# Performance work log

Measured on AMD Instinct MI355X. Metric: run time of the kernel, lower is better.

The kernel has to match this reference:

```python
import jax, jax.numpy as jnp
import numpy as np

N_RAYS = 131072
N_NODES = 524288
ENC_DEPTH = 8
ENC_DIM = 16
N_POINTS = 8
IN_DIM = N_POINTS * ENC_DEPTH * ENC_DIM  # 1024
INNER = 64


def setup_inputs() -> dict:
    key = jax.random.key(0)
    ks = jax.random.split(key, 9)
    orig = jax.random.uniform(ks[0], (N_RAYS, 3), dtype=jnp.float32)
    end = jax.random.uniform(ks[1], (N_RAYS, 3), dtype=jnp.float32)
    history = jax.random.randint(ks[2], (N_RAYS, ENC_DEPTH), 0, N_NODES, dtype=jnp.int32).astype(jnp.int64)
    nodes_min = jax.random.uniform(ks[3], (N_NODES, 3), dtype=jnp.float32)
    # extents strictly positive (module replaces 0 extents with 0.5)
    nodes_extent = jax.random.uniform(ks[4], (N_NODES, 3), dtype=jnp.float32) + 0.1
    emb = jax.random.normal(ks[5], (N_NODES, 8 * ENC_DIM), dtype=jnp.float32) * 0.1
    W1 = jax.random.normal(ks[6], (IN_DIM, INNER), dtype=jnp.float32) * (1.0 / np.sqrt(IN_DIM))
    W2 = jax.random.normal(ks[7], (INNER, INNER), dtype=jnp.float32) * (1.0 / np.sqrt(INNER))
    W3 = jax.random.normal(ks[8], (INNER, 2), dtype=jnp.float32) * (1.0 / np.sqrt(INNER))
    return {"orig": orig, "end": end, "history": history, "nodes_min": nodes_min,
            "nodes_extent": nodes_extent, "emb": emb, "W1": W1, "W2": W2, "W3": W3}


def _net_forward(orig, end, history, nodes_min, nodes_extent, emb, W1, W2, W3):
    n = orig.shape[0]
    d = history.shape[1]
    # gather per-ray, per-depth node data (irregular access)
    nmin = nodes_min[history]          # (n, d, 3)
    ext = nodes_extent[history]        # (n, d, 3)
    po = jnp.clip((orig[:, None, :] - nmin) / ext, 0.0, 1.0)  # (n, d, 3)
    pe = jnp.clip((end[:, None, :] - nmin) / ext, 0.0, 1.0)
    ts = jnp.linspace(0.0, 1.0, N_POINTS, dtype=orig.dtype)
    pts = po[:, :, None, :] + (pe - po)[:, :, None, :] * ts[None, None, :, None]  # (n, d, P, 3)
    xd, yd, zd = pts[..., 0], pts[..., 1], pts[..., 2]
    # corner weights in the same order as bbox_feature.chunk(8): 000,100,010,001,101,011,110,111
    w = jnp.stack([
        (1 - xd) * (1 - yd) * (1 - zd),
        xd * (1 - yd) * (1 - zd),
        (1 - xd) * yd * (1 - zd),
        (1 - xd) * (1 - yd) * zd,
        xd * (1 - yd) * zd,
        (1 - xd) * yd * zd,
        xd * yd * (1 - zd),
        xd * yd * zd,
    ], axis=-1)                                    # (n, d, P, 8)
    corners = emb[history].reshape(n, d, 8, ENC_DIM)  # (n, d, 8, F)
    feat = jnp.einsum('ndpk,ndkf->ndpf', w, corners)  # (n, d, P, F)
    feat = feat.reshape(n, d * N_POINTS * ENC_DIM)    # concat over depth
    h = jax.nn.relu(feat @ W1)
    h = jax.nn.relu(h @ W2)
    a = h @ W3                                        # (n, 2)
    lengths = jnp.linalg.norm(end - orig, axis=-1)
    pred_cls = a[:, 0]
    pred_dist = a[:, 1] * lengths
    return jnp.stack([pred_cls, pred_dist], axis=-1)  # (n, 2)


def reference(orig, end, history, nodes_min, nodes_extent, emb, W1, W2, W3):
    return _net_forward(orig, end, history, nodes_min, nodes_extent, emb, W1, W2, W3)
```

## Files before the change

kernel.cpp:

```cpp
#include <hip/hip_runtime.h>
#include <cstdint>

#define ENC_DEPTH 8
#define RPB 64
#define THREADS 512

typedef __attribute__((ext_vector_type(8))) short bf16x8;
typedef __attribute__((ext_vector_type(4))) float f32x4;

union bf8u { bf16x8 v; unsigned u[4]; };

__device__ __forceinline__ unsigned short f2bf(float x) {
    union { float f; unsigned u; } v; v.f = x;
    unsigned r = v.u + 0x7fffu + ((v.u >> 16) & 1u);
    return (unsigned short)(r >> 16);
}
__device__ __forceinline__ float bf2f(unsigned short h) {
    union { unsigned u; float f; } v; v.u = ((unsigned)h) << 16;
    return v.f;
}
__device__ __forceinline__ unsigned cvtpk(float lo, float hi) {
    unsigned r;
    asm volatile("v_cvt_pk_bf16_f32 %0, %1, %2" : "=v"(r) : "v"(lo), "v"(hi));
    return r;
}
__device__ __forceinline__ float clamp01(float x) { return fminf(fmaxf(x, 0.f), 1.f); }

__global__ void w1t_pre(const float* __restrict__ W1, unsigned short* __restrict__ W1T) {
    int tid = blockIdx.x * 256 + threadIdx.x;
    int col = tid >> 7, kb = tid & 127;
    const float* src = W1 + (size_t)kb * 512 + col;
    bf8u r;
    #pragma unroll
    for (int j = 0; j < 4; ++j)
        r.u[j] = cvtpk(src[(2 * j) * 64], src[(2 * j + 1) * 64]);
    *(bf16x8*)(W1T + (size_t)col * 1024 + kb * 8) = r.v;
}

template<bool GW>
__global__ __launch_bounds__(THREADS, GW ? 5 : 4) void nbvh_kernel(
    const float* __restrict__ orig, const float* __restrict__ endp,
    const int* __restrict__ hist, const float* __restrict__ nodes_min,
    const float* __restrict__ nodes_extent, const float* __restrict__ emb,
    const float* __restrict__ W1, const unsigned short* __restrict__ W1T,
    const float* __restrict__ W2, const float* __restrict__ W3,
    float* __restrict__ out)
{
    __shared__ int hist_s[RPB * ENC_DEPTH];
    __shared__ __align__(16) unsigned short corners_s[64 * 136];
    __shared__ __align__(16) unsigned short feat_s[64 * 136];
    __shared__ __align__(16) unsigned short w1t_s[64 * 136];

    const int t = threadIdx.x;
    const int r0 = blockIdx.x * RPB;
    const int wave = t >> 6, lane = t & 63;
    const int rayl = t >> 3, kc = t & 7;

    hist_s[t] = hist[r0 * ENC_DEPTH + t];

    const float* opr = orig + (size_t)(r0 + rayl) * 3;
    const float* epr = endp + (size_t)(r0 + rayl) * 3;
    float oex = opr[0], oey = opr[1], oez = opr[2];
    float eex = epr[0], eey = epr[1], eez = epr[2];

    asm volatile("s_waitcnt lgkmcnt(0)" ::: "memory");

    int node = hist_s[rayl << 3];
    const float4* ep0 = (const float4*)(emb + ((size_t)node << 7) + (kc << 4));
    float4 pf0 = ep0[0], pf1 = ep0[1], pf2 = ep0[2], pf3 = ep0[3];
    float nm0 = nodes_min[node * 3], nm1 = nodes_min[node * 3 + 1], nm2 = nodes_min[node * 3 + 2];
    float ex0 = nodes_extent[node * 3], ex1 = nodes_extent[node * 3 + 1], ex2 = nodes_extent[node * 3 + 2];

    f32x4 acc0 = {0.f, 0.f, 0.f, 0.f};
    f32x4 acc1 = {0.f, 0.f, 0.f, 0.f};
    const int m0 = (wave >> 1) * 16;
    const int n0 = (wave & 1) * 32;
    const float tt = (float)kc * (1.0f / 7.0f);

    float nn0 = 0.f, nn1 = 0.f, nn2 = 0.f, en0 = 0.f, en1 = 0.f, en2 = 0.f;

    for (int d = 0; d < ENC_DEPTH; ++d) {
        bf16x8 wtl0, wtl1;
        float wfa[16];
        if constexpr (GW) {
            const unsigned short* wp = W1T + (size_t)rayl * 1024 + d * 128 + (kc << 4);
            wtl0 = *(const bf16x8*)wp;
            wtl1 = *(const bf16x8*)(wp + 8);
        } else {
            const float* wp = W1 + (size_t)(d * 128 + (kc << 4)) * 64 + rayl;
            #pragma unroll
            for (int j = 0; j < 16; ++j) wfa[j] = wp[j << 6];
        }

        {
            bf8u c0, c1;
            c0.u[0] = cvtpk(pf0.x, pf0.y); c0.u[1] = cvtpk(pf0.z, pf0.w);
            c0.u[2] = cvtpk(pf1.x, pf1.y); c0.u[3] = cvtpk(pf1.z, pf1.w);
            c1.u[0] = cvtpk(pf2.x, pf2.y); c1.u[1] = cvtpk(pf2.z, pf2.w);
            c1.u[2] = cvtpk(pf3.x, pf3.y); c1.u[3] = cvtpk(pf3.z, pf3.w);
            unsigned short* cb = corners_s + rayl * 136 + (kc << 4);
            *(bf16x8*)cb = c0.v;
            *(bf16x8*)(cb + 8) = c1.v;
        }

        if (d < ENC_DEPTH - 1) {
            int node1 = hist_s[(rayl << 3) + d + 1];
            const float4* ep2 = (const float4*)(emb + ((size_t)node1 << 7) + (kc << 4));
            pf0 = ep2[0]; pf1 = ep2[1]; pf2 = ep2[2]; pf3 = ep2[3];
            nn0 = nodes_min[node1 * 3]; nn1 = nodes_min[node1 * 3 + 1]; nn2 = nodes_min[node1 * 3 + 2];
            en0 = nodes_extent[node1 * 3]; en1 = nodes_extent[node1 * 3 + 1]; en2 = nodes_extent[node1 * 3 + 2];
        }

        if constexpr (GW) {
            unsigned short* wb = w1t_s + rayl * 136 + (kc << 4);
            *(bf16x8*)wb = wtl0;
            *(bf16x8*)(wb + 8) = wtl1;
        } else {
            bf8u a0, a1;
            #pragma unroll
            for (int j = 0; j < 4; ++j) {
                a0.u[j] = cvtpk(wfa[2 * j], wfa[2 * j + 1]);
                a1.u[j] = cvtpk(wfa[8 + 2 * j], wfa[9 + 2 * j]);
            }
            unsigned short* wb = w1t_s + rayl * 136 + (kc << 4);
            *(bf16x8*)wb = a0.v;
            *(bf16x8*)(wb + 8) = a1.v;
        }

        {
            float rx = __builtin_amdgcn_rcpf(ex0);
            float ry = __builtin_amdgcn_rcpf(ex1);
            float rz = __builtin_amdgcn_rcpf(ex2);
            float po0 = clamp01((oex - nm0) * rx);
            float po1 = clamp01((oey - nm1) * ry);
            float po2 = clamp01((oez - nm2) * rz);
            float pe0 = clamp01((eex - nm0) * rx);
            float pe1 = clamp01((eey - nm1) * ry);
            float pe2 = clamp01((eez - nm2) * rz);
            float x = po0 + (pe0 - po0) * tt;
            float y = po1 + (pe1 - po1) * tt;
            float z = po2 + (pe2 - po2) * tt;
            float ox = 1.f - x, oy = 1.f - y, oz = 1.f - z;
            float w[8];
            w[0] = ox * oy * oz;  w[1] = x * oy * oz;
            w[2] = ox * y * oz;   w[3] = ox * oy * z;
            w[4] = x * oy * z;    w[5] = ox * y * z;
            w[6] = x * y * oz;    w[7] = x * y * z;

            const unsigned short* cbase = corners_s + rayl * 136;
            bf8u f0v, f1v;
            {
                float fa[8];
                #pragma unroll
                for (int f = 0; f < 8; ++f) fa[f] = 0.f;
                #pragma unroll
                for (int k = 0; k < 8; ++k) {
                    bf16x8 cv = *(const bf16x8*)(cbase + (k << 4));
                    #pragma unroll
                    for (int f = 0; f < 8; ++f)
                        fa[f] = fmaf(w[k], bf2f((unsigned short)cv[f]), fa[f]);
                }
                #pragma unroll
                for (int j = 0; j < 4; ++j) f0v.u[j] = cvtpk(fa[2 * j], fa[2 * j + 1]);
            }
            {
                float fb_[8];
                #pragma unroll
                for (int f = 0; f < 8; ++f) fb_[f] = 0.f;
                #pragma unroll
                for (int k = 0; k < 8; ++k) {
                    bf16x8 cv = *(const bf16x8*)(cbase + (k << 4) + 8);
                    #pragma unroll
                    for (int f = 0; f < 8; ++f)
                        fb_[f] = fmaf(w[k], bf2f((unsigned short)cv[f]), fb_[f]);
                }
                #pragma unroll
                for (int j = 0; j < 4; ++j) f1v.u[j] = cvtpk(fb_[2 * j], fb_[2 * j + 1]);
            }
            unsigned short* fbp = feat_s + rayl * 136 + (kc << 4);
            *(bf16x8*)fbp = f0v.v;
            *(bf16x8*)(fbp + 8) = f1v.v;
        }

        asm volatile("s_waitcnt lgkmcnt(0)" ::: "memory");
        __builtin_amdgcn_s_barrier();
        asm volatile("" ::: "memory");

        {
            int q = lane >> 4, c = lane & 15;
            #pragma unroll
            for (int kk = 0; kk < 4; ++kk) {
                int koff = kk * 32 + q * 8;
                bf16x8 af = *(const bf16x8*)(feat_s + (m0 + c) * 136 + koff);
                bf16x8 b0 = *(const bf16x8*)(w1t_s + (n0 + c) * 136 + koff);
                bf16x8 b1 = *(const bf16x8*)(w1t_s + (n0 + 16 + c) * 136 + koff);
                acc0 = __builtin_amdgcn_mfma_f32_16x16x32_bf16(af, b0, acc0, 0, 0, 0);
                acc1 = __builtin_amdgcn_mfma_f32_16x16x32_bf16(af, b1, acc1, 0, 0, 0);
            }
        }

        asm volatile("s_waitcnt lgkmcnt(0)" ::: "memory");
        __builtin_amdgcn_s_barrier();
        asm volatile("" ::: "memory");

        nm0 = nn0; nm1 = nn1; nm2 = nn2;
        ex0 = en0; ex1 = en1; ex2 = en2;
    }

    float* h1s = (float*)feat_s;
    {
        int colb = lane & 15, rq = (lane >> 4) << 2;
        #pragma unroll
        for (int r = 0; r < 4; ++r) {
            h1s[(m0 + rq + r) * 68 + n0 + colb]      = fmaxf(acc0[r], 0.f);
            h1s[(m0 + rq + r) * 68 + n0 + 16 + colb] = fmaxf(acc1[r], 0.f);
        }
    }
    float* w2s = (float*)w1t_s;
    {
        int row = t >> 3, cgr8 = (t & 7) << 3;
        const float4* wr = (const float4*)(W2 + (row << 6) + cgr8);
        float4 wa = wr[0], wbv = wr[1];
        *(float4*)(w2s + row * 68 + cgr8) = wa;
        *(float4*)(w2s + row * 68 + cgr8 + 4) = wbv;
    }
    asm volatile("s_waitcnt lgkmcnt(0)" ::: "memory");
    __builtin_amdgcn_s_barrier();
    asm volatile("" ::: "memory");

    float* h2s = (float*)corners_s;
    {
        int tp4 = (t & 7) << 2;
        float slo0 = 0.f, slo1 = 0.f, slo2 = 0.f, slo3 = 0.f;
        float shi0 = 0.f, shi1 = 0.f, shi2 = 0.f, shi3 = 0.f;
        const float* hr = h1s + rayl * 68;
        #pragma unroll
        for (int i4 = 0; i4 < 16; ++i4) {
            float4 hv = *(const float4*)(hr + (i4 << 2));
            #pragma unroll
            for (int s = 0; s < 4; ++s) {
                float h = (s == 0) ? hv.x : (s == 1) ? hv.y : (s == 2) ? hv.z : hv.w;
                const float* wrow = w2s + (i4 * 4 + s) * 68;
                float4 wlo = *(const float4*)(wrow + tp4);
                float4 whi = *(const float4*)(wrow + 32 + tp4);
                slo0 = fmaf(h, wlo.x, slo0); slo1 = fmaf(h, wlo.y, slo1);
                slo2 = fmaf(h, wlo.z, slo2); slo3 = fmaf(h, wlo.w, slo3);
                shi0 = fmaf(h, whi.x, shi0); shi1 = fmaf(h, whi.y, shi1);
                shi2 = fmaf(h, whi.z, shi2); shi3 = fmaf(h, whi.w, shi3);
            }
        }
        float4 rlo; rlo.x = fmaxf(slo0, 0.f); rlo.y = fmaxf(slo1, 0.f);
        rlo.z = fmaxf(slo2, 0.f); rlo.w = fmaxf(slo3, 0.f);
        float4 rhi; rhi.x = fmaxf(shi0, 0.f); rhi.y = fmaxf(shi1, 0.f);
        rhi.z = fmaxf(shi2, 0.f); rhi.w = fmaxf(shi3, 0.f);
        *(float4*)(h2s + rayl * 68 + tp4) = rlo;
        *(float4*)(h2s + rayl * 68 + 32 + tp4) = rhi;
    }
    asm volatile("s_waitcnt lgkmcnt(0)" ::: "memory");
    __builtin_amdgcn_s_barrier();
    asm volatile("" ::: "memory");

    if (t < 128) {
        int ray2 = t >> 1, c = t & 1;
        const float* hr = h2s + ray2 * 68;
        float a = 0.f;
        #pragma unroll
        for (int i4 = 0; i4 < 16; ++i4) {
            float4 hv = *(const float4*)(hr + (i4 << 2));
            const float4* w3p = (const float4*)(W3 + (i4 << 3));
            float4 wa = w3p[0], wbv = w3p[1];
            if (c == 0) {
                a = fmaf(hv.x, wa.x, a); a = fmaf(hv.y, wa.z, a);
                a = fmaf(hv.z, wbv.x, a); a = fmaf(hv.w, wbv.z, a);
            } else {
                a = fmaf(hv.x, wa.y, a); a = fmaf(hv.y, wa.w, a);
                a = fmaf(hv.z, wbv.y, a); a = fmaf(hv.w, wbv.w, a);
            }
        }
        if (c) {
            const float* o2p = orig + (size_t)(r0 + ray2) * 3;
            const float* e2p = endp + (size_t)(r0 + ray2) * 3;
            float dx = e2p[0] - o2p[0], dy = e2p[1] - o2p[1], dz = e2p[2] - o2p[2];
            a *= sqrtf(dx * dx + dy * dy + dz * dz);
        }
        out[((r0 + ray2) << 1) + c] = a;
    }
}

extern "C" void kernel_launch(void* const* d_in, const int* in_sizes, int n_in,
                              void* d_out, int out_size, void* d_ws, size_t ws_size,
                              hipStream_t stream) {
    const float* orig = (const float*)d_in[0];
    const float* endp = (const float*)d_in[1];
    const int*   hist = (const int*)d_in[2];
    const float* nmin = (const float*)d_in[3];
    const float* next = (const float*)d_in[4];
    const float* emb  = (const float*)d_in[5];
    const float* W1   = (const float*)d_in[6];
    const float* W2   = (const float*)d_in[7];
    const float* W3   = (const float*)d_in[8];
    float* out = (float*)d_out;
    const int n_rays = in_sizes[0] / 3;
    dim3 grid(n_rays / RPB);

    const size_t w1t_bytes = (size_t)64 * 1024 * sizeof(unsigned short);
    if (ws_size >= w1t_bytes && d_ws != nullptr) {
        unsigned short* W1T = (unsigned short*)d_ws;
        w1t_pre<<<dim3(32), dim3(256), 0, stream>>>(W1, W1T);
        nbvh_kernel<true><<<grid, THREADS, 0, stream>>>(orig, endp, hist, nmin, next,
                                                        emb, W1, W1T, W2, W3, out);
    } else {
        nbvh_kernel<false><<<grid, THREADS, 0, stream>>>(orig, endp, hist, nmin, next,
                                                         emb, W1, nullptr, W2, W3, out);
    }
}
```

Measured before the change: 520.3 us.

## Make each wave own 16 rays end-to-end, removing block barriers and W1 staging

The kernel is reorganised so each 64-lane wave handles 16 rays for the whole pipeline: gather, trilinear interpolation, the W1 MFMA for all 64 outputs, then the W2 and W3 layers. Because every wave touches only its own rows of shared memory, all block-wide barriers are replaced by wave-local waitcnt/sched_barrier, and W1 fragments are read straight from global or L2 instead of being staged in LDS. The block drops to 256 threads and the hist/w1t shared buffers are removed. In exchange each wave now loads all W1 columns and reads W2 from global per lane, which adds memory traffic and register pressure.

```diff
diff --git a/kernel.cpp b/kernel.cpp
--- a/kernel.cpp
+++ b/kernel.cpp
@@ -3,26 +3,21 @@
 
 #define ENC_DEPTH 8
 #define RPB 64
-#define THREADS 512
+#define THREADS 256
 
 typedef __attribute__((ext_vector_type(8))) short bf16x8;
 typedef __attribute__((ext_vector_type(4))) float f32x4;
 
 union bf8u { bf16x8 v; unsigned u[4]; };
 
-__device__ __forceinline__ unsigned short f2bf(float x) {
-    union { float f; unsigned u; } v; v.f = x;
-    unsigned r = v.u + 0x7fffu + ((v.u >> 16) & 1u);
-    return (unsigned short)(r >> 16);
-}
-__device__ __forceinline__ float bf2f(unsigned short h) {
-    union { unsigned u; float f; } v; v.u = ((unsigned)h) << 16;
-    return v.f;
-}
 __device__ __forceinline__ unsigned cvtpk(float lo, float hi) {
     unsigned r;
     asm volatile("v_cvt_pk_bf16_f32 %0, %1, %2" : "=v"(r) : "v"(lo), "v"(hi));
     return r;
+}
+__device__ __forceinline__ float bf2f(unsigned short h) {
+    union { unsigned u; float f; } v; v.u = ((unsigned)h) << 16;
+    return v.f;
 }
 __device__ __forceinline__ float clamp01(float x) { return fminf(fmaxf(x, 0.f), 1.f); }
 
@@ -38,7 +33,7 @@
 }
 
 template<bool GW>
-__global__ __launch_bounds__(THREADS, GW ? 5 : 4) void nbvh_kernel(
+__global__ __launch_bounds__(THREADS, 4) void nbvh_kernel(
     const float* __restrict__ orig, const float* __restrict__ endp,
     const int* __restrict__ hist, const float* __restrict__ nodes_min,
     const float* __restrict__ nodes_extent, const float* __restrict__ emb,
@@ -46,86 +41,67 @@
     const float* __restrict__ W2, const float* __restrict__ W3,
     float* __restrict__ out)
 {
-    __shared__ int hist_s[RPB * ENC_DEPTH];
     __shared__ __align__(16) unsigned short corners_s[64 * 136];
     __shared__ __align__(16) unsigned short feat_s[64 * 136];
-    __shared__ __align__(16) unsigned short w1t_s[64 * 136];
 
     const int t = threadIdx.x;
+    const int wave = t >> 6, lane = t & 63;
+    const int c = lane & 15;
+    const int s = lane >> 4;
+    const int ray = wave * 16 + c;
     const int r0 = blockIdx.x * RPB;
-    const int wave = t >> 6, lane = t & 63;
-    const int rayl = t >> 3, kc = t & 7;
-
-    hist_s[t] = hist[r0 * ENC_DEPTH + t];
-
-    const float* opr = orig + (size_t)(r0 + rayl) * 3;
-    const float* epr = endp + (size_t)(r0 + rayl) * 3;
+    const int gray = r0 + ray;
+
+    const int* hrow_g = hist + (size_t)gray * ENC_DEPTH;
+
+    const float* opr = orig + (size_t)gray * 3;
+    const float* epr = endp + (size_t)gray * 3;
     float oex = opr[0], oey = opr[1], oez = opr[2];
     float eex = epr[0], eey = epr[1], eez = epr[2];
 
-    asm volatile("s_waitcnt lgkmcnt(0)" ::: "memory");
-
-    int node = hist_s[rayl << 3];
-    const float4* ep0 = (const float4*)(emb + ((size_t)node << 7) + (kc << 4));
-    float4 pf0 = ep0[0], pf1 = ep0[1], pf2 = ep0[2], pf3 = ep0[3];
-    float nm0 = nodes_min[node * 3], nm1 = nodes_min[node * 3 + 1], nm2 = nodes_min[node * 3 + 2];
-    float ex0 = nodes_extent[node * 3], ex1 = nodes_extent[node * 3 + 1], ex2 = nodes_extent[node * 3 + 2];
-
-    f32x4 acc0 = {0.f, 0.f, 0.f, 0.f};
-    f32x4 acc1 = {0.f, 0.f, 0.f, 0.f};
-    const int m0 = (wave >> 1) * 16;
-    const int n0 = (wave & 1) * 32;
-    const float tt = (float)kc * (1.0f / 7.0f);
-
-    float nn0 = 0.f, nn1 = 0.f, nn2 = 0.f, en0 = 0.f, en1 = 0.f, en2 = 0.f;
+    int node0 = hrow_g[0];
+    const float4* eb = (const float4*)(emb + ((size_t)node0 << 7)) + s * 8;
+    float4 p0 = eb[0], p1 = eb[1], p2 = eb[2], p3 = eb[3];
+    float4 p4 = eb[4], p5 = eb[5], p6 = eb[6], p7 = eb[7];
+    float nm0 = nodes_min[node0 * 3], nm1 = nodes_min[node0 * 3 + 1], nm2 = nodes_min[node0 * 3 + 2];
+    float ex0 = nodes_extent[node0 * 3], ex1 = nodes_extent[node0 * 3 + 1], ex2 = nodes_extent[node0 * 3 + 2];
+
+    f32x4 acc0 = {0.f,0.f,0.f,0.f}, acc1 = {0.f,0.f,0.f,0.f};
+    f32x4 acc2 = {0.f,0.f,0.f,0.f}, acc3 = {0.f,0.f,0.f,0.f};
+
+    const float ttA = (float)s * (1.0f / 7.0f);
+    const float ttB = (float)(s + 4) * (1.0f / 7.0f);
 
     for (int d = 0; d < ENC_DEPTH; ++d) {
-        bf16x8 wtl0, wtl1;
-        float wfa[16];
-        if constexpr (GW) {
-            const unsigned short* wp = W1T + (size_t)rayl * 1024 + d * 128 + (kc << 4);
-            wtl0 = *(const bf16x8*)wp;
-            wtl1 = *(const bf16x8*)(wp + 8);
-        } else {
-            const float* wp = W1 + (size_t)(d * 128 + (kc << 4)) * 64 + rayl;
-            #pragma unroll
-            for (int j = 0; j < 16; ++j) wfa[j] = wp[j << 6];
-        }
-
         {
-            bf8u c0, c1;
-            c0.u[0] = cvtpk(pf0.x, pf0.y); c0.u[1] = cvtpk(pf0.z, pf0.w);
-            c0.u[2] = cvtpk(pf1.x, pf1.y); c0.u[3] = cvtpk(pf1.z, pf1.w);
-            c1.u[0] = cvtpk(pf2.x, pf2.y); c1.u[1] = cvtpk(pf2.z, pf2.w);
-            c1.u[2] = cvtpk(pf3.x, pf3.y); c1.u[3] = cvtpk(pf3.z, pf3.w);
-            unsigned short* cb = corners_s + rayl * 136 + (kc << 4);
-            *(bf16x8*)cb = c0.v;
-            *(bf16x8*)(cb + 8) = c1.v;
-        }
-
+            bf8u w0, w1v, w2v, w3v;
+            w0.u[0] = cvtpk(p0.x, p0.y); w0.u[1] = cvtpk(p0.z, p0.w);
+            w0.u[2] = cvtpk(p1.x, p1.y); w0.u[3] = cvtpk(p1.z, p1.w);
+            w1v.u[0] = cvtpk(p2.x, p2.y); w1v.u[1] = cvtpk(p2.z, p2.w);
+            w1v.u[2] = cvtpk(p3.x, p3.y); w1v.u[3] = cvtpk(p3.z, p3.w);
+            w2v.u[0] = cvtpk(p4.x, p4.y); w2v.u[1] = cvtpk(p4.z, p4.w);
+            w2v.u[2] = cvtpk(p5.x, p5.y); w2v.u[3] = cvtpk(p5.z, p5.w);
+            w3v.u[0] = cvtpk(p6.x, p6.y); w3v.u[1] = cvtpk(p6.z, p6.w);
+            w3v.u[2] = cvtpk(p7.x, p7.y); w3v.u[3] = cvtpk(p7.z, p7.w);
+            unsigned short* cbp = corners_s + ray * 136 + s * 32;
+            *(bf16x8*)cbp        = w0.v;
+            *(bf16x8*)(cbp + 8)  = w1v.v;
+            *(bf16x8*)(cbp + 16) = w2v.v;
+            *(bf16x8*)(cbp + 24) = w3v.v;
+        }
+
+        float nn0 = nm0, nn1 = nm1, nn2 = nm2, en0 = ex0, en1 = ex1, en2 = ex2;
         if (d < ENC_DEPTH - 1) {
-            int node1 = hist_s[(rayl << 3) + d + 1];
-            const float4* ep2 = (const float4*)(emb + ((size_t)node1 << 7) + (kc << 4));
-            pf0 = ep2[0]; pf1 = ep2[1]; pf2 = ep2[2]; pf3 = ep2[3];
+            int node1 = hrow_g[d + 1];
+            const float4* eb2 = (const float4*)(emb + ((size_t)node1 << 7)) + s * 8;
+            p0 = eb2[0]; p1 = eb2[1]; p2 = eb2[2]; p3 = eb2[3];
+            p4 = eb2[4]; p5 = eb2[5]; p6 = eb2[6]; p7 = eb2[7];
             nn0 = nodes_min[node1 * 3]; nn1 = nodes_min[node1 * 3 + 1]; nn2 = nodes_min[node1 * 3 + 2];
             en0 = nodes_extent[node1 * 3]; en1 = nodes_extent[node1 * 3 + 1]; en2 = nodes_extent[node1 * 3 + 2];
         }
 
-        if constexpr (GW) {
-            unsigned short* wb = w1t_s + rayl * 136 + (kc << 4);
-            *(bf16x8*)wb = wtl0;
-            *(bf16x8*)(wb + 8) = wtl1;
-        } else {
-            bf8u a0, a1;
-            #pragma unroll
-            for (int j = 0; j < 4; ++j) {
-                a0.u[j] = cvtpk(wfa[2 * j], wfa[2 * j + 1]);
-                a1.u[j] = cvtpk(wfa[8 + 2 * j], wfa[9 + 2 * j]);
-            }
-            unsigned short* wb = w1t_s + rayl * 136 + (kc << 4);
-            *(bf16x8*)wb = a0.v;
-            *(bf16x8*)(wb + 8) = a1.v;
-        }
+        asm volatile("s_waitcnt lgkmcnt(0)" ::: "memory");
+        __builtin_amdgcn_sched_barrier(0);
 
         {
             float rx = __builtin_amdgcn_rcpf(ex0);
@@ -137,139 +113,144 @@
             float pe0 = clamp01((eex - nm0) * rx);
             float pe1 = clamp01((eey - nm1) * ry);
             float pe2 = clamp01((eez - nm2) * rz);
-            float x = po0 + (pe0 - po0) * tt;
-            float y = po1 + (pe1 - po1) * tt;
-            float z = po2 + (pe2 - po2) * tt;
-            float ox = 1.f - x, oy = 1.f - y, oz = 1.f - z;
-            float w[8];
-            w[0] = ox * oy * oz;  w[1] = x * oy * oz;
-            w[2] = ox * y * oz;   w[3] = ox * oy * z;
-            w[4] = x * oy * z;    w[5] = ox * y * z;
-            w[6] = x * y * oz;    w[7] = x * y * z;
-
-            const unsigned short* cbase = corners_s + rayl * 136;
-            bf8u f0v, f1v;
-            {
-                float fa[8];
-                #pragma unroll
-                for (int f = 0; f < 8; ++f) fa[f] = 0.f;
+            float d0 = pe0 - po0, d1 = pe1 - po1, d2 = pe2 - po2;
+            const unsigned short* cbase = corners_s + ray * 136;
+
+            #pragma unroll
+            for (int pr = 0; pr < 2; ++pr) {
+                float ttv = pr ? ttB : ttA;
+                float x = po0 + d0 * ttv;
+                float y = po1 + d1 * ttv;
+                float z = po2 + d2 * ttv;
+                float ox = 1.f - x, oy = 1.f - y, oz = 1.f - z;
+                float w[8];
+                w[0] = ox * oy * oz;  w[1] = x * oy * oz;
+                w[2] = ox * y * oz;   w[3] = ox * oy * z;
+                w[4] = x * oy * z;    w[5] = ox * y * z;
+                w[6] = x * y * oz;    w[7] = x * y * z;
+                float fa[16];
+                #pragma unroll
+                for (int f = 0; f < 16; ++f) fa[f] = 0.f;
                 #pragma unroll
                 for (int k = 0; k < 8; ++k) {
-                    bf16x8 cv = *(const bf16x8*)(cbase + (k << 4));
+                    bf16x8 cv0 = *(const bf16x8*)(cbase + (k << 4));
+                    bf16x8 cv1 = *(const bf16x8*)(cbase + (k << 4) + 8);
                     #pragma unroll
-                    for (int f = 0; f < 8; ++f)
-                        fa[f] = fmaf(w[k], bf2f((unsigned short)cv[f]), fa[f]);
+                    for (int f = 0; f < 8; ++f) {
+                        fa[f]     = fmaf(w[k], bf2f((unsigned short)cv0[f]), fa[f]);
+                        fa[f + 8] = fmaf(w[k], bf2f((unsigned short)cv1[f]), fa[f + 8]);
+                    }
                 }
-                #pragma unroll
-                for (int j = 0; j < 4; ++j) f0v.u[j] = cvtpk(fa[2 * j], fa[2 * j + 1]);
-            }
-            {
-                float fb_[8];
-                #pragma unroll
-                for (int f = 0; f < 8; ++f) fb_[f] = 0.f;
-                #pragma unroll
-                for (int k = 0; k < 8; ++k) {
-                    bf16x8 cv = *(const bf16x8*)(cbase + (k << 4) + 8);
-                    #pragma unroll
-                    for (int f = 0; f < 8; ++f)
-                        fb_[f] = fmaf(w[k], bf2f((unsigned short)cv[f]), fb_[f]);
+                bf8u fv0, fv1;
+                #pragma unroll
+                for (int j = 0; j < 4; ++j) {
+                    fv0.u[j] = cvtpk(fa[2 * j], fa[2 * j + 1]);
+                    fv1.u[j] = cvtpk(fa[8 + 2 * j], fa[9 + 2 * j]);
                 }
-                #pragma unroll
-                for (int j = 0; j < 4; ++j) f1v.u[j] = cvtpk(fb_[2 * j], fb_[2 * j + 1]);
-            }
-            unsigned short* fbp = feat_s + rayl * 136 + (kc << 4);
-            *(bf16x8*)fbp = f0v.v;
-            *(bf16x8*)(fbp + 8) = f1v.v;
+                unsigned short* fbp = feat_s + ray * 136 + ((pr ? s + 4 : s) << 4);
+                *(bf16x8*)fbp = fv0.v;
+                *(bf16x8*)(fbp + 8) = fv1.v;
+            }
         }
 
         asm volatile("s_waitcnt lgkmcnt(0)" ::: "memory");
-        __builtin_amdgcn_s_barrier();
-        asm volatile("" ::: "memory");
-
-        {
-            int q = lane >> 4, c = lane & 15;
+        __builtin_amdgcn_sched_barrier(0);
+
+        #pragma unroll
+        for (int kk = 0; kk < 4; ++kk) {
+            bf16x8 af = *(const bf16x8*)(feat_s + ray * 136 + kk * 32 + s * 8);
+            bf16x8 b0, b1, b2, b3;
+            if constexpr (GW) {
+                const unsigned short* wb = W1T + (size_t)c * 1024 + d * 128 + kk * 32 + s * 8;
+                b0 = *(const bf16x8*)wb;
+                b1 = *(const bf16x8*)(wb + 16 * 1024);
+                b2 = *(const bf16x8*)(wb + 32 * 1024);
+                b3 = *(const bf16x8*)(wb + 48 * 1024);
+            } else {
+                const float* wsrc = W1 + (size_t)(d * 128 + kk * 32 + s * 8) * 64 + c;
+                bf8u t0, t1, t2, t3;
+                #pragma unroll
+                for (int j = 0; j < 4; ++j) {
+                    t0.u[j] = cvtpk(wsrc[(2*j)*64],      wsrc[(2*j+1)*64]);
+                    t1.u[j] = cvtpk(wsrc[(2*j)*64 + 16], wsrc[(2*j+1)*64 + 16]);
+                    t2.u[j] = cvtpk(wsrc[(2*j)*64 + 32], wsrc[(2*j+1)*64 + 32]);
+                    t3.u[j] = cvtpk(wsrc[(2*j)*64 + 48], wsrc[(2*j+1)*64 + 48]);
+                }
+                b0 = t0.v; b1 = t1.v; b2 = t2.v; b3 = t3.v;
+            }
+            acc0 = __builtin_amdgcn_mfma_f32_16x16x32_bf16(af, b0, acc0, 0, 0, 0);
+            acc1 = __builtin_amdgcn_mfma_f32_16x16x32_bf16(af, b1, acc1, 0, 0, 0);
+            acc2 = __builtin_amdgcn_mfma_f32_16x16x32_bf16(af, b2, acc2, 0, 0, 0);
+            acc3 = __builtin_amdgcn_mfma_f32_16x16x32_bf16(af, b3, acc3, 0, 0, 0);
+        }
+
+        nm0 = nn0; nm1 = nn1; nm2 = nn2;
+        ex0 = en0; ex1 = en1; ex2 = en2;
+    }
+
+    float* h1s = (float*)feat_s;
+    {
+        int rb = wave * 16 + (s << 2);
+        #pragma unroll
+        for (int r = 0; r < 4; ++r) {
+            h1s[(rb + r) * 68 + 0  + c] = fmaxf(acc0[r], 0.f);
+            h1s[(rb + r) * 68 + 16 + c] = fmaxf(acc1[r], 0.f);
+            h1s[(rb + r) * 68 + 32 + c] = fmaxf(acc2[r], 0.f);
+            h1s[(rb + r) * 68 + 48 + c] = fmaxf(acc3[r], 0.f);
+        }
+    }
+    asm volatile("s_waitcnt lgkmcnt(0)" ::: "memory");
+    __builtin_amdgcn_sched_barrier(0);
+
+    float* h2s = (float*)corners_s;
+    {
+        float sa[16];
+        #pragma unroll
+        for (int j = 0; j < 16; ++j) sa[j] = 0.f;
+        const float* hr = h1s + (size_t)(wave * 16 + c) * 68;
+        #pragma unroll
+        for (int k4 = 0; k4 < 16; ++k4) {
+            float4 hv = *(const float4*)(hr + (k4 << 2));
             #pragma unroll
             for (int kk = 0; kk < 4; ++kk) {
-                int koff = kk * 32 + q * 8;
-                bf16x8 af = *(const bf16x8*)(feat_s + (m0 + c) * 136 + koff);
-                bf16x8 b0 = *(const bf16x8*)(w1t_s + (n0 + c) * 136 + koff);
-                bf16x8 b1 = *(const bf16x8*)(w1t_s + (n0 + 16 + c) * 136 + koff);
-                acc0 = __builtin_amdgcn_mfma_f32_16x16x32_bf16(af, b0, acc0, 0, 0, 0);
-                acc1 = __builtin_amdgcn_mfma_f32_16x16x32_bf16(af, b1, acc1, 0, 0, 0);
-            }
-        }
-
-        asm volatile("s_waitcnt lgkmcnt(0)" ::: "memory");
-        __builtin_amdgcn_s_barrier();
-        asm volatile("" ::: "memory");
-
-        nm0 = nn0; nm1 = nn1; nm2 = nn2;
-        ex0 = en0; ex1 = en1; ex2 = en2;
-    }
-
-    float* h1s = (float*)feat_s;
-    {
-        int colb = lane & 15, rq = (lane >> 4) << 2;
-        #pragma unroll
-        for (int r = 0; r < 4; ++r) {
-            h1s[(m0 + rq + r) * 68 + n0 + colb]      = fmaxf(acc0[r], 0.f);
-            h1s[(m0 + rq + r) * 68 + n0 + 16 + colb] = fmaxf(acc1[r], 0.f);
-        }
-    }
-    float* w2s = (float*)w1t_s;
-    {
-        int row = t >> 3, cgr8 = (t & 7) << 3;
-        const float4* wr = (const float4*)(W2 + (row << 6) + cgr8);
-        float4 wa = wr[0], wbv = wr[1];
-        *(float4*)(w2s + row * 68 + cgr8) = wa;
-        *(float4*)(w2s + row * 68 + cgr8 + 4) = wbv;
+                float h = (kk == 0) ? hv.x : (kk == 1) ? hv.y : (kk == 2) ? hv.z : hv.w;
+                const float4* wr = (const float4*)(W2 + (size_t)(k4 * 4 + kk) * 64 + s * 16);
+                float4 wv0 = wr[0], wv1 = wr[1], wv2 = wr[2], wv3 = wr[3];
+                sa[0]  = fmaf(h, wv0.x, sa[0]);  sa[1]  = fmaf(h, wv0.y, sa[1]);
+                sa[2]  = fmaf(h, wv0.z, sa[2]);  sa[3]  = fmaf(h, wv0.w, sa[3]);
+                sa[4]  = fmaf(h, wv1.x, sa[4]);  sa[5]  = fmaf(h, wv1.y, sa[5]);
+                sa[6]  = fmaf(h, wv1.z, sa[6]);  sa[7]  = fmaf(h, wv1.w, sa[7]);
+                sa[8]  = fmaf(h, wv2.x, sa[8]);  sa[9]  = fmaf(h, wv2.y, sa[9]);
+                sa[10] = fmaf(h, wv2.z, sa[10]); sa[11] = fmaf(h, wv2.w, sa[11]);
+                sa[12] = fmaf(h, wv3.x, sa[12]); sa[13] = fmaf(h, wv3.y, sa[13]);
+                sa[14] = fmaf(h, wv3.z, sa[14]); sa[15] = fmaf(h, wv3.w, sa[15]);
+            }
+        }
+        float* hb = h2s + (size_t)(wave * 16 + c) * 68 + s * 16;
+        #pragma unroll
+        for (int j4 = 0; j4 < 4; ++j4) {
+            float4 rv;
+            rv.x = fmaxf(sa[4 * j4 + 0], 0.f);
+            rv.y = fmaxf(sa[4 * j4 + 1], 0.f);
+            rv.z = fmaxf(sa[4 * j4 + 2], 0.f);
+            rv.w = fmaxf(sa[4 * j4 + 3], 0.f);
+            *(float4*)(hb + 4 * j4) = rv;
+        }
     }
     asm volatile("s_waitcnt lgkmcnt(0)" ::: "memory");
-    __builtin_amdgcn_s_barrier();
-    asm volatile("" ::: "memory");
-
-    float* h2s = (float*)corners_s;
-    {
-        int tp4 = (t & 7) << 2;
-        float slo0 = 0.f, slo1 = 0.f, slo2 = 0.f, slo3 = 0.f;
-        float shi0 = 0.f, shi1 = 0.f, shi2 = 0.f, shi3 = 0.f;
-        const float* hr = h1s + rayl * 68;
+    __builtin_amdgcn_sched_barrier(0);
+
+    if (lane < 32) {
+        int rr = lane >> 1, cc2 = lane & 1;
+        int lrow = wave * 16 + rr;
+        const float* hr2 = h2s + (size_t)lrow * 68;
+        float a = 0.f;
         #pragma unroll
         for (int i4 = 0; i4 < 16; ++i4) {
-            float4 hv = *(const float4*)(hr + (i4 << 2));
-            #pragma unroll
-            for (int s = 0; s < 4; ++s) {
-                float h = (s == 0) ? hv.x : (s == 1) ? hv.y : (s == 2) ? hv.z : hv.w;
-                const float* wrow = w2s + (i4 * 4 + s) * 68;
-                float4 wlo = *(const float4*)(wrow + tp4);
-                float4 whi = *(const float4*)(wrow + 32 + tp4);
-                slo0 = fmaf(h, wlo.x, slo0); slo1 = fmaf(h, wlo.y, slo1);
-                slo2 = fmaf(h, wlo.z, slo2); slo3 = fmaf(h, wlo.w, slo3);
-                shi0 = fmaf(h, whi.x, shi0); shi1 = fmaf(h, whi.y, shi1);
-                shi2 = fmaf(h, whi.z, shi2); shi3 = fmaf(h, whi.w, shi3);
-            }
-        }
-        float4 rlo; rlo.x = fmaxf(slo0, 0.f); rlo.y = fmaxf(slo1, 0.f);
-        rlo.z = fmaxf(slo2, 0.f); rlo.w = fmaxf(slo3, 0.f);
-        float4 rhi; rhi.x = fmaxf(shi0, 0.f); rhi.y = fmaxf(shi1, 0.f);
-        rhi.z = fmaxf(shi2, 0.f); rhi.w = fmaxf(shi3, 0.f);
-        *(float4*)(h2s + rayl * 68 + tp4) = rlo;
-        *(float4*)(h2s + rayl * 68 + 32 + tp4) = rhi;
-    }
-    asm volatile("s_waitcnt lgkmcnt(0)" ::: "memory");
-    __builtin_amdgcn_s_barrier();
-    asm volatile("" ::: "memory");
-
-    if (t < 128) {
-        int ray2 = t >> 1, c = t & 1;
-        const float* hr = h2s + ray2 * 68;
-        float a = 0.f;
-        #pragma unroll
-        for (int i4 = 0; i4 < 16; ++i4) {
-            float4 hv = *(const float4*)(hr + (i4 << 2));
+            float4 hv = *(const float4*)(hr2 + (i4 << 2));
             const float4* w3p = (const float4*)(W3 + (i4 << 3));
             float4 wa = w3p[0], wbv = w3p[1];
-            if (c == 0) {
+            if (cc2 == 0) {
                 a = fmaf(hv.x, wa.x, a); a = fmaf(hv.y, wa.z, a);
                 a = fmaf(hv.z, wbv.x, a); a = fmaf(hv.w, wbv.z, a);
             } else {
@@ -277,13 +258,13 @@
                 a = fmaf(hv.z, wbv.y, a); a = fmaf(hv.w, wbv.w, a);
             }
         }
-        if (c) {
-            const float* o2p = orig + (size_t)(r0 + ray2) * 3;
-            const float* e2p = endp + (size_t)(r0 + ray2) * 3;
+        if (cc2) {
+            const float* o2p = orig + (size_t)(r0 + lrow) * 3;
+            const float* e2p = endp + (size_t)(r0 + lrow) * 3;
             float dx = e2p[0] - o2p[0], dy = e2p[1] - o2p[1], dz = e2p[2] - o2p[2];
             a *= sqrtf(dx * dx + dy * dy + dz * dz);
         }
-        out[((r0 + ray2) << 1) + c] = a;
+        out[((size_t)(r0 + lrow) << 1) + cc2] = a;
     }
 }
 
```

New measurement: 591.5 us. 1.14x slower.
